# Performance work log

Hardware: AMD Instinct MI355X
Metric: run time of the kernel (lower is better)

The kernel has to match this reference:

```python
import jax, jax.numpy as jnp
import numpy as np

BANDS = np.array([0, 1, 2, 3, 4])
LOG_STDEVS = (0.0, 1.0)
CLAHE_MIN_STDEV = 1.0
K = 9      # CLAHE kernel size (hardcoded in module)
PAD = 4    # CLAHE reflect padding (hardcoded in module)


def _box_mean(x):
    # x: [B, C, H, W]; mean over KxK sliding window with reflect padding,
    # identical math to torch Unfold + mean over the K*K window axis.
    p = jnp.pad(x, ((0, 0), (0, 0), (PAD, PAD), (PAD, PAD)), mode='reflect')
    s = jax.lax.reduce_window(p, jnp.float32(0.0), jax.lax.add,
                              (1, 1, K, K), (1, 1, 1, 1), 'VALID')
    return s / (K * K)


def _clahe(img5d, min_stdev):
    # img5d: [B, C, 1, H, W]
    x = img5d[:, :, 0]
    res = x - _box_mean(x)
    stdev = jnp.sqrt(_box_mean(res * res))
    return (res / jnp.maximum(stdev, min_stdev))[:, :, None]


def setup_inputs() -> dict:
    key = jax.random.key(0)
    k1, k2 = jax.random.split(key, 2)
    B, C, H, W = 8, 5, 512, 512
    T = 3
    images = jax.random.normal(k1, (B, C, H, W), jnp.float32) * 10.0 + 100.0
    # background must be positive (asserted > 1e-6 in the module)
    background = jax.random.uniform(k2, (B, C, H, W), jnp.float32) * 50.0 + 50.0
    # learnable asinh params, initialized exactly as in __init__
    asinh_thresholds = jnp.tile(
        jnp.array([0.0, 1.0, 10.0], jnp.float32).reshape(1, 1, T, 1, 1),
        (1, C, 1, 1, 1))
    asinh_scales = jnp.full((1, C, T, 1, 1), np.log(0.1), jnp.float32)
    return {'images': images, 'background': background,
            'asinh_thresholds': asinh_thresholds, 'asinh_scales': asinh_scales}


def reference(images, background, asinh_thresholds, asinh_scales):
    raw = images[:, BANDS][:, :, None]        # [B, C, 1, H, W]
    bg = background[:, BANDS][:, :, None]     # [B, C, 1, H, W]
    inputs = [raw]                            # include_original=True; asinh on -> no raw background channel
    for t in LOG_STDEVS:
        off = (raw - bg) / jnp.sqrt(bg) - t
        inputs.append(jnp.log(jnp.maximum(off + 1.0, 1.0)))
    inputs.append(_clahe(raw, CLAHE_MIN_STDEV))
    inputs.append(jnp.arcsinh((raw - asinh_thresholds) * jnp.exp(asinh_scales)))
    return jnp.concatenate(inputs, axis=2)    # [B, C, 7, H, W]
```

## Files before the change

### kernel.cpp

```cpp
#include <hip/hip_runtime.h>
#include <math.h>

#define IMG_H 512
#define IMG_W 512
#define TS 32
#define NC 5
#define NB 8

__device__ __forceinline__ int reflect_idx(int i, int n) {
    if (i < 0) i = -i;
    if (i >= n) i = 2 * n - 2 - i;
    return i;
}

__device__ __forceinline__ float fast_log(float x) {
    return __builtin_amdgcn_logf(x) * 0.6931471805599453f;
}

__device__ __forceinline__ float fast_asinh(float v) {
    float a = fabsf(v);
    float r = fast_log(a + __builtin_amdgcn_sqrtf(fmaf(a, a, 1.0f)));
    return copysignf(r, v);
}

__global__ __launch_bounds__(256)
void imnorm_kernel(const float* __restrict__ img, const float* __restrict__ bgr,
                   const float* __restrict__ thr, const float* __restrict__ scl,
                   float* __restrict__ out)
{
    const int plane = blockIdx.z;
    const int c = plane % NC;
    const int bx = blockIdx.x;
    const int t = threadIdx.y * 32 + threadIdx.x;
    const size_t chs = (size_t)IMG_H * IMG_W;
    float* op = out + (size_t)plane * 7 * chs;

    if (bx >= 16) {
        const int w0s = (bx - 16) * TS;
        const int h0s = blockIdx.y * TS;
        const int row = t >> 3;
        const int col = (t & 7) * 4;

        const size_t base = (size_t)plane * chs + (size_t)(h0s + row) * IMG_W + (w0s + col);
        const float4 raw4 = *reinterpret_cast<const float4*>(img + base);
        const float4 bg4  = *reinterpret_cast<const float4*>(bgr + base);

        float s_thr[3], s_exp[3];
        #pragma unroll
        for (int j = 0; j < 3; ++j) {
            s_thr[j] = thr[c * 3 + j];
            s_exp[j] = __builtin_amdgcn_exp2f(scl[c * 3 + j] * 1.4426950408889634f);
        }

        const float rawa[4] = {raw4.x, raw4.y, raw4.z, raw4.w};
        const float bga[4]  = {bg4.x,  bg4.y,  bg4.z,  bg4.w};
        float o_l0[4], o_l1[4], o_a0[4], o_a1[4], o_a2[4];
        #pragma unroll
        for (int j = 0; j < 4; ++j) {
            float raw  = rawa[j];
            float off0 = (raw - bga[j]) * __builtin_amdgcn_rsqf(bga[j]);
            o_l0[j] = fast_log(fmaxf(off0 + 1.0f, 1.0f));
            o_l1[j] = fast_log(fmaxf(off0, 1.0f));
            o_a0[j] = fast_asinh((raw - s_thr[0]) * s_exp[0]);
            o_a1[j] = fast_asinh((raw - s_thr[1]) * s_exp[1]);
            o_a2[j] = fast_asinh((raw - s_thr[2]) * s_exp[2]);
        }

        float* p = op + (size_t)(h0s + row) * IMG_W + (w0s + col);
        *reinterpret_cast<float4*>(p) = raw4;
        *reinterpret_cast<float4*>(p + 1 * chs) = make_float4(o_l0[0], o_l0[1], o_l0[2], o_l0[3]);
        *reinterpret_cast<float4*>(p + 2 * chs) = make_float4(o_l1[0], o_l1[1], o_l1[2], o_l1[3]);
        *reinterpret_cast<float4*>(p + 4 * chs) = make_float4(o_a0[0], o_a0[1], o_a0[2], o_a0[3]);
        *reinterpret_cast<float4*>(p + 5 * chs) = make_float4(o_a1[0], o_a1[1], o_a1[2], o_a1[3]);
        *reinterpret_cast<float4*>(p + 6 * chs) = make_float4(o_a2[0], o_a2[1], o_a2[2], o_a2[3]);
        return;
    }

    const int h0 = blockIdx.y * TS;
    const int w0 = bx * TS;
    const bool edge_w = (w0 == 0) || (w0 + TS == IMG_W);
    const bool edge_h = (h0 == 0) || (h0 + TS == IMG_H);

    const float* x = img + (size_t)plane * chs;

    __shared__ float xs[48][52];
    __shared__ float rs[40][44];
    __shared__ float pool[48 * 41];
    float (*h1)[41] = reinterpret_cast<float (*)[41]>(pool);
    float (*v2)[44] = reinterpret_cast<float (*)[44]>(pool);

    if (!edge_w && !edge_h) {
        const float4* src4 = reinterpret_cast<const float4*>(
            x + (size_t)(h0 - 8) * IMG_W + (w0 - 8));
        #pragma unroll
        for (int k = 0; k < 3; ++k) {
            int i = t + k * 256;
            if (i < 576) {
                int r = i / 12, cc = i - r * 12;
                *reinterpret_cast<float4*>(&xs[r][cc * 4]) = src4[r * 128 + cc];
            }
        }
    } else {
        #pragma unroll
        for (int k = 0; k < 9; ++k) {
            int i = t + k * 256;
            int r = i / 48, cc = i - r * 48;
            int gr = reflect_idx(h0 - 8 + r, IMG_H);
            int gc = reflect_idx(w0 - 8 + cc, IMG_W);
            xs[r][cc] = x[gr * IMG_W + gc];
        }
    }
    __syncthreads();

    if (t < 240) {
        const int r  = t / 5;
        const int c0 = (t - r * 5) * 8;
        float s = xs[r][c0];
        #pragma unroll
        for (int d = 1; d < 9; ++d) s += xs[r][c0 + d];
        h1[r][c0] = s;
        #pragma unroll
        for (int k = 1; k < 8; ++k) {
            s += xs[r][c0 + 8 + k] - xs[r][c0 + k - 1];
            h1[r][c0 + k] = s;
        }
    }
    __syncthreads();

    if (t < 200) {
        const int seg = t / 40;
        const int cl  = t - seg * 40;
        const int r0  = seg * 8;
        float s = h1[r0][cl];
        #pragma unroll
        for (int d = 1; d < 9; ++d) s += h1[r0 + d][cl];
        rs[r0][cl] = xs[r0 + 4][cl + 4] - s * (1.0f / 81.0f);
        #pragma unroll
        for (int k = 1; k < 8; ++k) {
            s += h1[r0 + 8 + k][cl] - h1[r0 + k - 1][cl];
            rs[r0 + k][cl] = xs[r0 + k + 4][cl + 4] - s * (1.0f / 81.0f);
        }
    }
    __syncthreads();

    if (t < 160) {
        const int seg = t / 40;
        const int cl  = t - seg * 40;
        const int r0  = seg * 8;
        if (!edge_h) {
            float v = rs[r0][cl];
            float s = v * v;
            #pragma unroll
            for (int d = 1; d < 9; ++d) { v = rs[r0 + d][cl]; s = fmaf(v, v, s); }
            v2[r0][cl] = s;
            #pragma unroll
            for (int k = 1; k < 8; ++k) {
                float a = rs[r0 + 8 + k][cl];
                float b = rs[r0 + k - 1][cl];
                s = fmaf(a, a, fmaf(b, -b, s));
                v2[r0 + k][cl] = s;
            }
        } else {
            #pragma unroll
            for (int k = 0; k < 8; ++k) {
                const int hh = h0 + r0 + k;
                float s = 0.f;
                #pragma unroll
                for (int d = 0; d < 9; ++d) {
                    int mr = reflect_idx(hh - 4 + d, IMG_H) - (h0 - 4);
                    float v = rs[mr][cl];
                    s = fmaf(v, v, s);
                }
                v2[r0 + k][cl] = s;
            }
        }
    }
    __syncthreads();

    const int r5  = t >> 3;
    const int wl0 = (t & 7) * 4;

    float ssum[4];
    if (!edge_w) {
        const float* vr = &v2[r5][wl0];
        float4 A  = *reinterpret_cast<const float4*>(vr);
        float4 Bv = *reinterpret_cast<const float4*>(vr + 4);
        float4 Cv = *reinterpret_cast<const float4*>(vr + 8);
        float s0 = ((A.x + A.y) + (A.z + A.w)) + ((Bv.x + Bv.y) + (Bv.z + Bv.w)) + Cv.x;
        ssum[0] = s0;
        ssum[1] = s0      - A.x + Cv.y;
        ssum[2] = ssum[1] - A.y + Cv.z;
        ssum[3] = ssum[2] - A.z + Cv.w;
    } else {
        #pragma unroll
        for (int j = 0; j < 4; ++j) {
            const int w = w0 + wl0 + j;
            float s = 0.f;
            #pragma unroll
            for (int d = 0; d < 9; ++d) {
                int mc = reflect_idx(w - 4 + d, IMG_W) - (w0 - 4);
                s += v2[r5][mc];
            }
            ssum[j] = s;
        }
    }

    const float4 rsv = *reinterpret_cast<const float4*>(&rs[r5 + 4][wl0 + 4]);
    const float rsa[4] = {rsv.x, rsv.y, rsv.z, rsv.w};
    float o_cl[4];
    #pragma unroll
    for (int j = 0; j < 4; ++j) {
        float stdev = __builtin_amdgcn_sqrtf(fmaxf(ssum[j], 0.0f) * (1.0f / 81.0f));
        o_cl[j] = rsa[j] * __builtin_amdgcn_rcpf(fmaxf(stdev, 1.0f));
    }

    float* p = op + 3 * chs + (size_t)(h0 + r5) * IMG_W + (w0 + wl0);
    *reinterpret_cast<float4*>(p) = make_float4(o_cl[0], o_cl[1], o_cl[2], o_cl[3]);
}

extern "C" void kernel_launch(void* const* d_in, const int* in_sizes, int n_in,
                              void* d_out, int out_size, void* d_ws, size_t ws_size,
                              hipStream_t stream) {
    const float* img = (const float*)d_in[0];
    const float* bg  = (const float*)d_in[1];
    const float* thr = (const float*)d_in[2];
    const float* scl = (const float*)d_in[3];
    float* out = (float*)d_out;

    dim3 grid(32, IMG_H / TS, NB * NC);
    dim3 block(32, 8);
    hipLaunchKernelGGL(imnorm_kernel, grid, block, 0, stream,
                       img, bg, thr, scl, out);
}
```

Before: 371.6 us.

## Split fused kernel into separate CLAHE and grid-strided elementwise stream kernels

```diff
diff --git a/kernel.cpp b/kernel.cpp
--- a/kernel.cpp
+++ b/kernel.cpp
@@ -6,6 +6,8 @@
 #define TS 32
 #define NC 5
 #define NB 8
+#define CHS (IMG_H * IMG_W)
+#define CHS4 (CHS / 4)
 
 __device__ __forceinline__ int reflect_idx(int i, int n) {
     if (i < 0) i = -i;
@@ -24,66 +26,18 @@
 }
 
 __global__ __launch_bounds__(256)
-void imnorm_kernel(const float* __restrict__ img, const float* __restrict__ bgr,
-                   const float* __restrict__ thr, const float* __restrict__ scl,
-                   float* __restrict__ out)
+void clahe_kernel(const float* __restrict__ img, float* __restrict__ out)
 {
     const int plane = blockIdx.z;
-    const int c = plane % NC;
-    const int bx = blockIdx.x;
-    const int t = threadIdx.y * 32 + threadIdx.x;
-    const size_t chs = (size_t)IMG_H * IMG_W;
-    float* op = out + (size_t)plane * 7 * chs;
-
-    if (bx >= 16) {
-        const int w0s = (bx - 16) * TS;
-        const int h0s = blockIdx.y * TS;
-        const int row = t >> 3;
-        const int col = (t & 7) * 4;
-
-        const size_t base = (size_t)plane * chs + (size_t)(h0s + row) * IMG_W + (w0s + col);
-        const float4 raw4 = *reinterpret_cast<const float4*>(img + base);
-        const float4 bg4  = *reinterpret_cast<const float4*>(bgr + base);
-
-        float s_thr[3], s_exp[3];
-        #pragma unroll
-        for (int j = 0; j < 3; ++j) {
-            s_thr[j] = thr[c * 3 + j];
-            s_exp[j] = __builtin_amdgcn_exp2f(scl[c * 3 + j] * 1.4426950408889634f);
-        }
-
-        const float rawa[4] = {raw4.x, raw4.y, raw4.z, raw4.w};
-        const float bga[4]  = {bg4.x,  bg4.y,  bg4.z,  bg4.w};
-        float o_l0[4], o_l1[4], o_a0[4], o_a1[4], o_a2[4];
-        #pragma unroll
-        for (int j = 0; j < 4; ++j) {
-            float raw  = rawa[j];
-            float off0 = (raw - bga[j]) * __builtin_amdgcn_rsqf(bga[j]);
-            o_l0[j] = fast_log(fmaxf(off0 + 1.0f, 1.0f));
-            o_l1[j] = fast_log(fmaxf(off0, 1.0f));
-            o_a0[j] = fast_asinh((raw - s_thr[0]) * s_exp[0]);
-            o_a1[j] = fast_asinh((raw - s_thr[1]) * s_exp[1]);
-            o_a2[j] = fast_asinh((raw - s_thr[2]) * s_exp[2]);
-        }
-
-        float* p = op + (size_t)(h0s + row) * IMG_W + (w0s + col);
-        *reinterpret_cast<float4*>(p) = raw4;
-        *reinterpret_cast<float4*>(p + 1 * chs) = make_float4(o_l0[0], o_l0[1], o_l0[2], o_l0[3]);
-        *reinterpret_cast<float4*>(p + 2 * chs) = make_float4(o_l1[0], o_l1[1], o_l1[2], o_l1[3]);
-        *reinterpret_cast<float4*>(p + 4 * chs) = make_float4(o_a0[0], o_a0[1], o_a0[2], o_a0[3]);
-        *reinterpret_cast<float4*>(p + 5 * chs) = make_float4(o_a1[0], o_a1[1], o_a1[2], o_a1[3]);
-        *reinterpret_cast<float4*>(p + 6 * chs) = make_float4(o_a2[0], o_a2[1], o_a2[2], o_a2[3]);
-        return;
-    }
-
     const int h0 = blockIdx.y * TS;
-    const int w0 = bx * TS;
+    const int w0 = blockIdx.x * TS;
     const bool edge_w = (w0 == 0) || (w0 + TS == IMG_W);
     const bool edge_h = (h0 == 0) || (h0 + TS == IMG_H);
 
-    const float* x = img + (size_t)plane * chs;
-
-    __shared__ float xs[48][52];
+    const float* x = img + (size_t)plane * CHS;
+    const int t = threadIdx.y * 32 + threadIdx.x;
+
+    __shared__ float xs[48][48];
     __shared__ float rs[40][44];
     __shared__ float pool[48 * 41];
     float (*h1)[41] = reinterpret_cast<float (*)[41]>(pool);
@@ -214,8 +168,63 @@
         o_cl[j] = rsa[j] * __builtin_amdgcn_rcpf(fmaxf(stdev, 1.0f));
     }
 
-    float* p = op + 3 * chs + (size_t)(h0 + r5) * IMG_W + (w0 + wl0);
+    float* p = out + ((size_t)plane * 7 + 3) * CHS + (size_t)(h0 + r5) * IMG_W + (w0 + wl0);
     *reinterpret_cast<float4*>(p) = make_float4(o_cl[0], o_cl[1], o_cl[2], o_cl[3]);
+}
+
+#define STREAM_BLOCKS 2560
+#define STREAM_ITERS  4
+
+__global__ __launch_bounds__(256)
+void stream_kernel(const float* __restrict__ img, const float* __restrict__ bgr,
+                   const float* __restrict__ thr, const float* __restrict__ scl,
+                   float* __restrict__ out)
+{
+    const int tid4 = blockIdx.x * 256 + threadIdx.x;
+    const int c = (tid4 >> 16) % NC;
+
+    float s_thr[3], s_exp[3];
+    #pragma unroll
+    for (int j = 0; j < 3; ++j) {
+        s_thr[j] = thr[c * 3 + j];
+        s_exp[j] = __builtin_amdgcn_exp2f(scl[c * 3 + j] * 1.4426950408889634f);
+    }
+
+    const float4* in4 = reinterpret_cast<const float4*>(img);
+    const float4* bg4 = reinterpret_cast<const float4*>(bgr);
+    float4* out4 = reinterpret_cast<float4*>(out);
+
+    #pragma unroll
+    for (int k = 0; k < STREAM_ITERS; ++k) {
+        const int idx4 = tid4 + k * (STREAM_BLOCKS * 256);
+        const int plane = idx4 >> 16;
+        const int within4 = idx4 & (CHS4 - 1);
+
+        const float4 raw4 = in4[idx4];
+        const float4 bgv4 = bg4[idx4];
+
+        const float rawa[4] = {raw4.x, raw4.y, raw4.z, raw4.w};
+        const float bga[4]  = {bgv4.x, bgv4.y, bgv4.z, bgv4.w};
+        float o_l0[4], o_l1[4], o_a0[4], o_a1[4], o_a2[4];
+        #pragma unroll
+        for (int j = 0; j < 4; ++j) {
+            float raw  = rawa[j];
+            float off0 = (raw - bga[j]) * __builtin_amdgcn_rsqf(bga[j]);
+            o_l0[j] = fast_log(fmaxf(off0 + 1.0f, 1.0f));
+            o_l1[j] = fast_log(fmaxf(off0, 1.0f));
+            o_a0[j] = fast_asinh((raw - s_thr[0]) * s_exp[0]);
+            o_a1[j] = fast_asinh((raw - s_thr[1]) * s_exp[1]);
+            o_a2[j] = fast_asinh((raw - s_thr[2]) * s_exp[2]);
+        }
+
+        float4* p = out4 + (size_t)plane * 7 * CHS4 + within4;
+        p[0 * CHS4] = raw4;
+        p[1 * CHS4] = make_float4(o_l0[0], o_l0[1], o_l0[2], o_l0[3]);
+        p[2 * CHS4] = make_float4(o_l1[0], o_l1[1], o_l1[2], o_l1[3]);
+        p[4 * CHS4] = make_float4(o_a0[0], o_a0[1], o_a0[2], o_a0[3]);
+        p[5 * CHS4] = make_float4(o_a1[0], o_a1[1], o_a1[2], o_a1[3]);
+        p[6 * CHS4] = make_float4(o_a2[0], o_a2[1], o_a2[2], o_a2[3]);
+    }
 }
 
 extern "C" void kernel_launch(void* const* d_in, const int* in_sizes, int n_in,
@@ -227,8 +236,8 @@
     const float* scl = (const float*)d_in[3];
     float* out = (float*)d_out;
 
-    dim3 grid(32, IMG_H / TS, NB * NC);
-    dim3 block(32, 8);
-    hipLaunchKernelGGL(imnorm_kernel, grid, block, 0, stream,
+    hipLaunchKernelGGL(clahe_kernel, dim3(IMG_W / TS, IMG_H / TS, NB * NC),
+                       dim3(32, 8), 0, stream, img, out);
+    hipLaunchKernelGGL(stream_kernel, dim3(STREAM_BLOCKS), dim3(256), 0, stream,
                        img, bg, thr, scl, out);
 }
```

Result: no change. 365.3 us (-1.7%).
